# Kernel optimization log

Measured on AMD Instinct MI355X. Metric: run time of the kernel, lower is better.

The kernel has to match this reference:

```python
import jax, jax.numpy as jnp
import numpy as np

IN_FEATURES = 4096
OUT_FEATURES = 4096
BLOCKSIZE = 64
FP4_CODEBOOK = np.array([0.0, 0.0052, 0.6667, 1.0, 0.3333, 0.5, 0.1667, 0.25,
                         0.0, -0.0052, -0.6667, -1.0, -0.3333, -0.5, -0.1667, -0.25],
                        dtype=np.float32)


def setup_inputs() -> dict:
    key = jax.random.key(0)
    k1, k2, k3, k4 = jax.random.split(key, 4)
    n_elements = OUT_FEATURES * IN_FEATURES
    n_blocks = n_elements // BLOCKSIZE
    x = jax.random.normal(k1, (4, 2048, IN_FEATURES), dtype=jnp.float32)
    weight_packed = jax.random.randint(k2, (n_elements // 2,), 0, 256, dtype=jnp.int32)
    scale = jax.random.uniform(k3, (n_blocks,), dtype=jnp.float32)
    bias = jax.random.normal(k4, (OUT_FEATURES,), dtype=jnp.float32)
    return {"x": x, "weight_packed": weight_packed, "scale": scale, "bias": bias}


def reference(x, weight_packed, scale, bias):
    codebook = jnp.asarray(FP4_CODEBOOK, dtype=x.dtype)
    # Unpack two 4-bit indices per byte: high nibble first, then low nibble.
    high = (weight_packed >> 4) & 15
    low = weight_packed & 15
    indices = jnp.stack([high, low], axis=1).reshape(-1)  # [n_elements]
    # LUT dequant + per-block scale broadcast.
    deq = codebook[indices].reshape(-1, BLOCKSIZE) * scale[:, None]  # [n_blocks, blocksize]
    weight = deq.reshape(OUT_FEATURES, IN_FEATURES)
    # F.linear(x, W, b) = x @ W.T + b
    return jnp.einsum('bsi,oi->bso', x, weight) + bias
```

## Files before the change

### kernel.cpp

```cpp
#include <hip/hip_runtime.h>
#include <stdint.h>
#include <stddef.h>

#define IN_F 4096
#define OUT_F 4096
#define M_TOT 8192

#define BM 128
#define BN 128
#define BK 64

#define BM2 256
#define BN2 256
#define BK2 64
#define NT2 (IN_F / BK2)

typedef __attribute__((ext_vector_type(8))) short short8;
typedef __attribute__((ext_vector_type(4))) float f32x4;
typedef __attribute__((ext_vector_type(4))) float float4v;
typedef __attribute__((ext_vector_type(4))) unsigned short u16x4;
typedef __attribute__((ext_vector_type(8))) unsigned short u16x8;
typedef unsigned short u16;

__constant__ float c_lut[16] = {
  0.0f, 0.0052f, 0.6667f, 1.0f, 0.3333f, 0.5f, 0.1667f, 0.25f,
  0.0f, -0.0052f, -0.6667f, -1.0f, -0.3333f, -0.5f, -0.1667f, -0.25f
};

__device__ __forceinline__ u16 f2bf(float f) {
  unsigned int x = __float_as_uint(f);
  x += 0x7fffu + ((x >> 16) & 1u);
  return (u16)(x >> 16);
}

__device__ __forceinline__ void gload_lds16(const u16* g, u16* lds) {
  __builtin_amdgcn_global_load_lds(
      (const __attribute__((address_space(1))) unsigned int*)g,
      (__attribute__((address_space(3))) unsigned int*)lds, 16, 0, 0);
}

#define BARRIER() do { asm volatile("" ::: "memory"); \
                       __builtin_amdgcn_s_barrier();  \
                       asm volatile("" ::: "memory"); } while (0)
#define LGW(n) do { asm volatile("s_waitcnt lgkmcnt(" #n ")" ::: "memory"); \
                    __builtin_amdgcn_sched_barrier(0); } while (0)
#define VMW(n) asm volatile("s_waitcnt vmcnt(" #n ")" ::: "memory")

__global__ __launch_bounds__(256) void k_prep(const float* __restrict__ x,
                                              u16* __restrict__ a,
                                              const int* __restrict__ wp,
                                              const float* __restrict__ scale,
                                              u16* __restrict__ b) {
  if (blockIdx.x < 512) {
    __shared__ float lut[16];
    if (threadIdx.x < 16) lut[threadIdx.x] = c_lut[threadIdx.x];
    __syncthreads();
    const int ng = (OUT_F * IN_F / 2) / 4;
    const int stride = 512 * 256;
    for (int t = blockIdx.x * 256 + threadIdx.x; t < ng; t += stride) {
      int4 p = ((const int4*)wp)[t];
      float s = scale[t >> 3];
      int by[4] = {p.x, p.y, p.z, p.w};
      u16x8 o;
#pragma unroll
      for (int q = 0; q < 4; ++q) {
        o[2 * q]     = f2bf(lut[(by[q] >> 4) & 15] * s);
        o[2 * q + 1] = f2bf(lut[by[q] & 15] * s);
      }
      ((u16x8*)b)[t] = o;
    }
  } else {
    const int n8 = (M_TOT * IN_F) / 8;
    const int stride = 4096 * 256;
    for (int t = (blockIdx.x - 512) * 256 + threadIdx.x; t < n8; t += stride) {
      float4v f0 = ((const float4v*)x)[2 * t];
      float4v f1 = ((const float4v*)x)[2 * t + 1];
      u16x8 o;
      o[0] = f2bf(f0.x); o[1] = f2bf(f0.y); o[2] = f2bf(f0.z); o[3] = f2bf(f0.w);
      o[4] = f2bf(f1.x); o[5] = f2bf(f1.y); o[6] = f2bf(f1.z); o[7] = f2bf(f1.w);
      ((u16x8*)a)[t] = o;
    }
  }
}


__device__ __forceinline__ void st_b(const u16* __restrict__ B, u16* dst,
                                     int nBase, int kt, int h, int k,
                                     int wave, int srow, int scol) {
  const int r0 = 64 * (wave >> 1) + 32 * h + 16 * k + 8 * (wave & 1);
  gload_lds16(B + (size_t)(nBase + r0 + srow) * IN_F + kt + scol, dst + r0 * BK2);
}
__device__ __forceinline__ void st_a(const u16* __restrict__ A, u16* dst,
                                     int mBase, int kt, int h, int k,
                                     int wave, int srow, int scol) {
  const int r0 = 128 * (wave >> 2) + 64 * h + 32 * k + 8 * (wave & 3);
  gload_lds16(A + (size_t)(mBase + r0 + srow) * IN_F + kt + scol, dst + r0 * BK2);
}

__device__ __forceinline__ void rd_b(short8 d[2][2], const u16* Bs_c, int bBase,
                                     int co0, int co1, int h) {
#pragma unroll
  for (int jj = 0; jj < 2; ++jj) {
    const int ro = bBase + (h * 2 + jj) * (16 * BK2);
    d[jj][0] = *(const short8*)&Bs_c[ro + co0];
    d[jj][1] = *(const short8*)&Bs_c[ro + co1];
  }
}
__device__ __forceinline__ void rd_a(short8 d[4][2], const u16* As_c, int aBase,
                                     int co0, int co1, int h) {
#pragma unroll
  for (int ii = 0; ii < 4; ++ii) {
    const int ro = aBase + (h * 4 + ii) * (16 * BK2);
    d[ii][0] = *(const short8*)&As_c[ro + co0];
    d[ii][1] = *(const short8*)&As_c[ro + co1];
  }
}
__device__ __forceinline__ void mma8(f32x4 acc[8][4], const short8 a[4][2],
                                     const short8 b[2][2], int i0, int j0) {
#pragma unroll
  for (int k2 = 0; k2 < 2; ++k2)
#pragma unroll
    for (int ii = 0; ii < 4; ++ii)
#pragma unroll
      for (int jj = 0; jj < 2; ++jj)
        acc[i0 + ii][j0 + jj] = __builtin_amdgcn_mfma_f32_16x16x32_bf16(
            a[ii][k2], b[jj][k2], acc[i0 + ii][j0 + jj], 0, 0, 0);
}

__global__ __launch_bounds__(512, 2) void k_gemm256(const u16* __restrict__ A,
                                                    const u16* __restrict__ B,
                                                    const float* __restrict__ bias,
                                                    float* __restrict__ C) {
  __shared__ u16 As[2][BM2 * BK2];
  __shared__ u16 Bs[2][BN2 * BK2];

  const int tid  = threadIdx.x;
  const int lane = tid & 63;
  const int wave = tid >> 6;

  const int bid   = blockIdx.x;
  const int xcd   = bid & 7;
  const int kk    = bid >> 3;
  const int tileM = (xcd >> 1) * 8 + (kk >> 3);
  const int tileN = (xcd & 1) * 8 + (kk & 7);
  const int mBase = tileM * BM2;
  const int nBase = tileN * BN2;

  const int wm = (wave >> 2) * 128;
  const int wn = (wave & 3) * 64;

  const int srow = lane >> 3;
  const int scol = ((lane & 7) ^ srow) * 8;

  const int frow = lane & 15;
  const int fx   = frow & 7;
  const int cq   = lane >> 4;
  const int co0  = ((cq ^ fx) << 3);
  const int co1  = (((4 + cq) ^ fx) << 3);
  const int aBase = (wm + frow) * BK2;
  const int bBase = (wn + frow) * BK2;

  f32x4 acc[8][4] = {};
  short8 aC[4][2], aN[4][2], b0[2][2], b1[2][2];

  st_a(A, As[0], mBase, 0, 0, 0, wave, srow, scol);
  st_a(A, As[0], mBase, 0, 0, 1, wave, srow, scol);
  st_b(B, Bs[0], nBase, 0, 0, 0, wave, srow, scol);
  st_b(B, Bs[0], nBase, 0, 0, 1, wave, srow, scol);
  st_b(B, Bs[0], nBase, 0, 1, 0, wave, srow, scol);
  st_b(B, Bs[0], nBase, 0, 1, 1, wave, srow, scol);
  st_a(A, As[0], mBase, 0, 1, 0, wave, srow, scol);
  st_a(A, As[0], mBase, 0, 1, 1, wave, srow, scol);
  st_a(A, As[1], mBase, BK2, 0, 0, wave, srow, scol);
  st_a(A, As[1], mBase, BK2, 0, 1, wave, srow, scol);
  VMW(2);
  BARRIER();
  rd_a(aC, As[0], aBase, co0, co1, 0);
  rd_b(b0, Bs[0], bBase, co0, co1, 0);

  for (int t = 0; t < NT2; ++t) {
    const int c = t & 1;
    u16* AsC = As[c];
    u16* BsC = Bs[c];
    u16* AsO = As[c ^ 1];
    u16* BsO = Bs[c ^ 1];
    const int kt1 = (t + 1) * BK2;
    const int kt2 = (t + 2) * BK2;

    rd_b(b1, BsC, bBase, co0, co1, 1);
    if (t + 1 < NT2) {
      st_b(B, BsO, nBase, kt1, 0, 0, wave, srow, scol);
      st_b(B, BsO, nBase, kt1, 0, 1, wave, srow, scol);
    }
    if (t < NT2 - 3) { VMW(4); } else { VMW(0); }
    BARRIER();
    LGW(4);
    __builtin_amdgcn_s_setprio(1);
    mma8(acc, aC, b0, 0, 0);
    __builtin_amdgcn_s_setprio(0);

    rd_a(aN, AsC, aBase, co0, co1, 1);
    if (t + 1 < NT2) {
      st_b(B, BsO, nBase, kt1, 1, 0, wave, srow, scol);
      st_b(B, BsO, nBase, kt1, 1, 1, wave, srow, scol);
    }
    if (t < NT2 - 3) { VMW(4); } else { VMW(0); }
    BARRIER();
    LGW(8);
    __builtin_amdgcn_s_setprio(1);
    mma8(acc, aC, b1, 0, 2);
    __builtin_amdgcn_s_setprio(0);

    if (t + 1 < NT2) rd_a(aC, AsO, aBase, co0, co1, 0);
    if (t + 1 < NT2) {
      st_a(A, AsO, mBase, kt1, 1, 0, wave, srow, scol);
      st_a(A, AsO, mBase, kt1, 1, 1, wave, srow, scol);
    }
    if (t < NT2 - 3) { VMW(4); } else { VMW(0); }
    BARRIER();
    if (t + 1 < NT2) { LGW(8); } else { LGW(0); }
    __builtin_amdgcn_s_setprio(1);
    mma8(acc, aN, b0, 4, 0);
    __builtin_amdgcn_s_setprio(0);

    if (t + 1 < NT2) rd_b(b0, BsO, bBase, co0, co1, 0);
    if (t + 2 < NT2) {
      st_a(A, AsC, mBase, kt2, 0, 0, wave, srow, scol);
      st_a(A, AsC, mBase, kt2, 0, 1, wave, srow, scol);
    }
    if (t < NT2 - 3) { VMW(4); } else { VMW(0); }
    BARRIER();
    __builtin_amdgcn_sched_barrier(0);
    __builtin_amdgcn_s_setprio(1);
    mma8(acc, aN, b1, 4, 2);
    __builtin_amdgcn_s_setprio(0);
  }

  const int ccol = lane & 15;
  const int crow = (lane >> 4) * 4;
#pragma unroll
  for (int j = 0; j < 4; ++j) {
    const int col = nBase + wn + j * 16 + ccol;
    const float bv = bias[col];
#pragma unroll
    for (int i = 0; i < 8; ++i) {
      const size_t rb = (size_t)(mBase + wm + i * 16 + crow) * OUT_F + col;
#pragma unroll
      for (int tt = 0; tt < 4; ++tt)
        C[rb + (size_t)tt * OUT_F] = acc[i][j][tt] + bv;
    }
  }
}

__global__ __launch_bounds__(256) void k_gemm_fused(const float* __restrict__ X,
                                                    const int* __restrict__ WP,
                                                    const float* __restrict__ scale,
                                                    const float* __restrict__ bias,
                                                    float* __restrict__ C) {
  __shared__ u16 As[BM * BK];
  __shared__ u16 Bs[BN * BK];
  __shared__ float lut[16];
  const int tid = threadIdx.x;
  if (tid < 16) lut[tid] = c_lut[tid];
  const int lane = tid & 63;
  const int wave = tid >> 6;
  const int mBase = blockIdx.y * BM;
  const int nBase = blockIdx.x * BN;
  const int wm = (wave >> 1) * 64;
  const int wn = (wave & 1) * 64;
  const int frow = lane & 15;
  const int fx   = lane & 7;
  const int cq   = lane >> 4;
  f32x4 acc[4][4] = {};
  __syncthreads();

  for (int kt = 0; kt < IN_F; kt += BK) {
#pragma unroll
    for (int i = 0; i < 8; ++i) {
      const int g = tid + i * 256;
      const int r = g >> 4, c = (g & 15) * 4;
      float4v f = *(const float4v*)&X[(size_t)(mBase + r) * IN_F + kt + c];
      u16x4 o;
      o.x = f2bf(f.x); o.y = f2bf(f.y); o.z = f2bf(f.z); o.w = f2bf(f.w);
      *(u16x4*)&As[r * BK + ((((c >> 3) ^ (r & 7)) << 3) | (c & 7))] = o;
    }
#pragma unroll
    for (int i = 0; i < 4; ++i) {
      const int g = tid + i * 256;
      const int r = g >> 3, c4 = (g & 7) * 4;
      int4 p = *(const int4*)&WP[(size_t)(nBase + r) * (IN_F / 2) + (kt >> 1) + c4];
      const float s = scale[(nBase + r) * 64 + (kt >> 6)];
      int by[4] = {p.x, p.y, p.z, p.w};
      u16x8 o;
#pragma unroll
      for (int q = 0; q < 4; ++q) {
        o[2 * q]     = f2bf(lut[(by[q] >> 4) & 15] * s);
        o[2 * q + 1] = f2bf(lut[by[q] & 15] * s);
      }
      *(u16x8*)&Bs[r * BK + (((g & 7) ^ (r & 7)) << 3)] = o;
    }
    __syncthreads();
#pragma unroll
    for (int ks = 0; ks < BK; ks += 32) {
      const int co = (((ks >> 3) + cq) ^ fx) << 3;
      short8 a[4], b[4];
#pragma unroll
      for (int i = 0; i < 4; ++i)
        a[i] = *(const short8*)&As[(wm + i * 16 + frow) * BK + co];
#pragma unroll
      for (int j = 0; j < 4; ++j)
        b[j] = *(const short8*)&Bs[(wn + j * 16 + frow) * BK + co];
#pragma unroll
      for (int i = 0; i < 4; ++i)
#pragma unroll
        for (int j = 0; j < 4; ++j)
          acc[i][j] = __builtin_amdgcn_mfma_f32_16x16x32_bf16(a[i], b[j], acc[i][j], 0, 0, 0);
    }
    __syncthreads();
  }

  const int ccol = lane & 15;
  const int crow = (lane >> 4) * 4;
#pragma unroll
  for (int j = 0; j < 4; ++j) {
    const int col = nBase + wn + j * 16 + ccol;
    const float bv = bias[col];
#pragma unroll
    for (int i = 0; i < 4; ++i) {
      const size_t rb = (size_t)(mBase + wm + i * 16 + crow) * OUT_F + col;
#pragma unroll
      for (int t = 0; t < 4; ++t)
        C[rb + (size_t)t * OUT_F] = acc[i][j][t] + bv;
    }
  }
}

extern "C" void kernel_launch(void* const* d_in, const int* in_sizes, int n_in,
                              void* d_out, int out_size, void* d_ws, size_t ws_size,
                              hipStream_t stream) {
  const float* x  = (const float*)d_in[0];
  const int*   wp = (const int*)d_in[1];
  const float* sc = (const float*)d_in[2];
  const float* bi = (const float*)d_in[3];
  float* out = (float*)d_out;

  const size_t bBytes = (size_t)OUT_F * IN_F * 2;
  const size_t aBytes = (size_t)M_TOT * IN_F * 2;

  if (ws_size >= aBytes + bBytes) {
    u16* B = (u16*)d_ws;
    u16* A = (u16*)((char*)d_ws + bBytes);
    k_prep<<<4608, 256, 0, stream>>>(x, A, wp, sc, B);
    k_gemm256<<<(M_TOT / BM2) * (OUT_F / BN2), 512, 0, stream>>>(A, B, bi, out);
  } else {
    dim3 grid(OUT_F / BN, M_TOT / BM);
    k_gemm_fused<<<grid, 256, 0, stream>>>(x, wp, sc, bi, out);
  }
}
```

Baseline: 518.0 us.

## Switch 256x256 GEMM to 32x32x16 bf16 MFMA with reworked LDS schedule

Replaces the 16x16x32 MFMA tiling in the main GEMM with 32x32x16 MFMAs, so each wave holds 4x2 32x32 accumulator tiles and reads its A and B fragments with a new swizzled LDS indexing. Larger MFMA tiles need fewer LDS fragment reads per flop and fewer instructions. The per-phase vmcnt waits and the order of LDS reads and global prefetches in the double-buffered loop are also reshuffled. The epilogue is rewritten for the 32x32 output layout, and the changed wait counts risk stalls or hazards if they are slightly off.

```diff
diff --git a/kernel.cpp b/kernel.cpp
--- a/kernel.cpp
+++ b/kernel.cpp
@@ -17,6 +17,7 @@
 
 typedef __attribute__((ext_vector_type(8))) short short8;
 typedef __attribute__((ext_vector_type(4))) float f32x4;
+typedef __attribute__((ext_vector_type(16))) float f32x16;
 typedef __attribute__((ext_vector_type(4))) float float4v;
 typedef __attribute__((ext_vector_type(4))) unsigned short u16x4;
 typedef __attribute__((ext_vector_type(8))) unsigned short u16x8;
@@ -97,34 +98,29 @@
   gload_lds16(A + (size_t)(mBase + r0 + srow) * IN_F + kt + scol, dst + r0 * BK2);
 }
 
-__device__ __forceinline__ void rd_b(short8 d[2][2], const u16* Bs_c, int bBase,
-                                     int co0, int co1, int h) {
-#pragma unroll
-  for (int jj = 0; jj < 2; ++jj) {
-    const int ro = bBase + (h * 2 + jj) * (16 * BK2);
-    d[jj][0] = *(const short8*)&Bs_c[ro + co0];
-    d[jj][1] = *(const short8*)&Bs_c[ro + co1];
-  }
-}
-__device__ __forceinline__ void rd_a(short8 d[4][2], const u16* As_c, int aBase,
-                                     int co0, int co1, int h) {
-#pragma unroll
-  for (int ii = 0; ii < 4; ++ii) {
-    const int ro = aBase + (h * 4 + ii) * (16 * BK2);
-    d[ii][0] = *(const short8*)&As_c[ro + co0];
-    d[ii][1] = *(const short8*)&As_c[ro + co1];
-  }
-}
-__device__ __forceinline__ void mma8(f32x4 acc[8][4], const short8 a[4][2],
-                                     const short8 b[2][2], int i0, int j0) {
-#pragma unroll
-  for (int k2 = 0; k2 < 2; ++k2)
-#pragma unroll
-    for (int ii = 0; ii < 4; ++ii)
-#pragma unroll
-      for (int jj = 0; jj < 2; ++jj)
-        acc[i0 + ii][j0 + jj] = __builtin_amdgcn_mfma_f32_16x16x32_bf16(
-            a[ii][k2], b[jj][k2], acc[i0 + ii][j0 + jj], 0, 0, 0);
+__device__ __forceinline__ void rd_b32(short8 d[4], const u16* Bs_c,
+                                       int bOff, int jhOff, int hx) {
+#pragma unroll
+  for (int ks = 0; ks < 4; ++ks)
+    d[ks] = *(const short8*)&Bs_c[bOff + jhOff + (((ks * 2) ^ hx) << 3)];
+}
+__device__ __forceinline__ void rd_a32(short8 d[2][4], const u16* As_c,
+                                       int aOff, int hOff, int hx) {
+#pragma unroll
+  for (int rb = 0; rb < 2; ++rb)
+#pragma unroll
+    for (int ks = 0; ks < 4; ++ks)
+      d[rb][ks] = *(const short8*)&As_c[aOff + hOff + rb * (32 * BK2) +
+                                        (((ks * 2) ^ hx) << 3)];
+}
+__device__ __forceinline__ void mma32(f32x16 acc[4][2], const short8 a[2][4],
+                                      const short8 b[4], int h, int jh) {
+#pragma unroll
+  for (int ks = 0; ks < 4; ++ks)
+#pragma unroll
+    for (int rb = 0; rb < 2; ++rb)
+      acc[h * 2 + rb][jh] = __builtin_amdgcn_mfma_f32_32x32x16_bf16(
+          a[rb][ks], b[ks], acc[h * 2 + rb][jh], 0, 0, 0);
 }
 
 __global__ __launch_bounds__(512, 2) void k_gemm256(const u16* __restrict__ A,
@@ -152,31 +148,25 @@
   const int srow = lane >> 3;
   const int scol = ((lane & 7) ^ srow) * 8;
 
-  const int frow = lane & 15;
-  const int fx   = frow & 7;
-  const int cq   = lane >> 4;
-  const int co0  = ((cq ^ fx) << 3);
-  const int co1  = (((4 + cq) ^ fx) << 3);
-  const int aBase = (wm + frow) * BK2;
-  const int bBase = (wn + frow) * BK2;
-
-  f32x4 acc[8][4] = {};
-  short8 aC[4][2], aN[4][2], b0[2][2], b1[2][2];
-
-  st_a(A, As[0], mBase, 0, 0, 0, wave, srow, scol);
-  st_a(A, As[0], mBase, 0, 0, 1, wave, srow, scol);
-  st_b(B, Bs[0], nBase, 0, 0, 0, wave, srow, scol);
-  st_b(B, Bs[0], nBase, 0, 0, 1, wave, srow, scol);
-  st_b(B, Bs[0], nBase, 0, 1, 0, wave, srow, scol);
-  st_b(B, Bs[0], nBase, 0, 1, 1, wave, srow, scol);
-  st_a(A, As[0], mBase, 0, 1, 0, wave, srow, scol);
-  st_a(A, As[0], mBase, 0, 1, 1, wave, srow, scol);
-  st_a(A, As[1], mBase, BK2, 0, 0, wave, srow, scol);
-  st_a(A, As[1], mBase, BK2, 0, 1, wave, srow, scol);
+  const int arow = lane & 31;
+  const int hx   = (lane >> 5) ^ (arow & 7);
+  const int aOff = (wm + arow) * BK2;
+  const int bOff = (wn + arow) * BK2;
+
+  f32x16 acc[4][2] = {};
+  short8 aC[2][4], aN[2][4], b0[4], b1[4];
+
+#define SA(dst, t, h, k) st_a(A, dst, mBase, (t) * BK2, h, k, wave, srow, scol)
+#define SB(dst, t, h, k) st_b(B, dst, nBase, (t) * BK2, h, k, wave, srow, scol)
+
+  SA(As[0], 0, 0, 0); SA(As[0], 0, 0, 1);
+  SB(Bs[0], 0, 0, 0); SB(Bs[0], 0, 0, 1);
+  SB(Bs[0], 0, 1, 0); SB(Bs[0], 0, 1, 1);
+  SA(As[0], 0, 1, 0); SA(As[0], 0, 1, 1);
+  SA(As[1], 1, 0, 0); SA(As[1], 1, 0, 1);
   VMW(2);
   BARRIER();
-  rd_a(aC, As[0], aBase, co0, co1, 0);
-  rd_b(b0, Bs[0], bBase, co0, co1, 0);
+  rd_a32(aC, As[0], aOff, 0, hx);
 
   for (int t = 0; t < NT2; ++t) {
     const int c = t & 1;
@@ -184,70 +174,68 @@
     u16* BsC = Bs[c];
     u16* AsO = As[c ^ 1];
     u16* BsO = Bs[c ^ 1];
-    const int kt1 = (t + 1) * BK2;
-    const int kt2 = (t + 2) * BK2;
-
-    rd_b(b1, BsC, bBase, co0, co1, 1);
+
+    if (t < NT2 - 1) { VMW(6); } else { VMW(0); }
+    rd_b32(b0, BsC, bOff, 0, hx);
+    __builtin_amdgcn_sched_barrier(0);
+    rd_b32(b1, BsC, bOff, 32 * BK2, hx);
     if (t + 1 < NT2) {
-      st_b(B, BsO, nBase, kt1, 0, 0, wave, srow, scol);
-      st_b(B, BsO, nBase, kt1, 0, 1, wave, srow, scol);
-    }
-    if (t < NT2 - 3) { VMW(4); } else { VMW(0); }
+      SB(BsO, t + 1, 0, 0); SB(BsO, t + 1, 0, 1);
+    }
     BARRIER();
     LGW(4);
     __builtin_amdgcn_s_setprio(1);
-    mma8(acc, aC, b0, 0, 0);
+    mma32(acc, aC, b0, 0, 0);
     __builtin_amdgcn_s_setprio(0);
 
-    rd_a(aN, AsC, aBase, co0, co1, 1);
+    rd_a32(aN, AsC, aOff, 64 * BK2, hx);
     if (t + 1 < NT2) {
-      st_b(B, BsO, nBase, kt1, 1, 0, wave, srow, scol);
-      st_b(B, BsO, nBase, kt1, 1, 1, wave, srow, scol);
-    }
-    if (t < NT2 - 3) { VMW(4); } else { VMW(0); }
+      SB(BsO, t + 1, 1, 0); SB(BsO, t + 1, 1, 1);
+    }
     BARRIER();
     LGW(8);
     __builtin_amdgcn_s_setprio(1);
-    mma8(acc, aC, b1, 0, 2);
+    mma32(acc, aC, b1, 0, 1);
     __builtin_amdgcn_s_setprio(0);
 
-    if (t + 1 < NT2) rd_a(aC, AsO, aBase, co0, co1, 0);
+    VMW(2);
     if (t + 1 < NT2) {
-      st_a(A, AsO, mBase, kt1, 1, 0, wave, srow, scol);
-      st_a(A, AsO, mBase, kt1, 1, 1, wave, srow, scol);
-    }
-    if (t < NT2 - 3) { VMW(4); } else { VMW(0); }
+      SA(AsO, t + 1, 1, 0); SA(AsO, t + 1, 1, 1);
+    }
     BARRIER();
     if (t + 1 < NT2) { LGW(8); } else { LGW(0); }
     __builtin_amdgcn_s_setprio(1);
-    mma8(acc, aN, b0, 4, 0);
+    mma32(acc, aN, b1, 1, 1);
     __builtin_amdgcn_s_setprio(0);
 
-    if (t + 1 < NT2) rd_b(b0, BsO, bBase, co0, co1, 0);
+    if (t + 1 < NT2) rd_a32(aC, AsO, aOff, 0, hx);
     if (t + 2 < NT2) {
-      st_a(A, AsC, mBase, kt2, 0, 0, wave, srow, scol);
-      st_a(A, AsC, mBase, kt2, 0, 1, wave, srow, scol);
-    }
-    if (t < NT2 - 3) { VMW(4); } else { VMW(0); }
+      SA(AsC, t + 2, 0, 0); SA(AsC, t + 2, 0, 1);
+    }
     BARRIER();
     __builtin_amdgcn_sched_barrier(0);
     __builtin_amdgcn_s_setprio(1);
-    mma8(acc, aN, b1, 4, 2);
+    mma32(acc, aN, b0, 1, 0);
     __builtin_amdgcn_s_setprio(0);
   }
 
-  const int ccol = lane & 15;
-  const int crow = (lane >> 4) * 4;
-#pragma unroll
-  for (int j = 0; j < 4; ++j) {
-    const int col = nBase + wn + j * 16 + ccol;
+#undef SA
+#undef SB
+
+  const int ccol = lane & 31;
+  const int rhi  = (lane >> 5) * 4;
+#pragma unroll
+  for (int j = 0; j < 2; ++j) {
+    const int col = nBase + wn + j * 32 + ccol;
     const float bv = bias[col];
 #pragma unroll
-    for (int i = 0; i < 8; ++i) {
-      const size_t rb = (size_t)(mBase + wm + i * 16 + crow) * OUT_F + col;
-#pragma unroll
-      for (int tt = 0; tt < 4; ++tt)
-        C[rb + (size_t)tt * OUT_F] = acc[i][j][tt] + bv;
+    for (int i = 0; i < 4; ++i) {
+      const int rbase = mBase + wm + i * 32 + rhi;
+#pragma unroll
+      for (int reg = 0; reg < 16; ++reg) {
+        const int row = rbase + (reg & 3) + 8 * (reg >> 2);
+        C[(size_t)row * OUT_F + col] = acc[i][j][reg] + bv;
+      }
     }
   }
 }
```

New measurement: 543.0 us. 4.8% more time.
